# Optimization experiments

Hardware: AMD Instinct MI355X
Metric: run time of the kernel (lower is better)

The kernel has to match this reference:

```python
import jax, jax.numpy as jnp
import numpy as np

NUM_CLASSES = 512  # P distinct identities in the batch (labels are in [0, P))
TAU = 0.5
EPS = 1e-12


def _l2norm(x):
    # F.normalize(x, dim=1) with eps clamp
    n = jnp.sqrt(jnp.sum(x * x, axis=1, keepdims=True))
    return x / jnp.maximum(n, EPS)


def setup_inputs() -> dict:
    key = jax.random.key(0)
    k1, k2, k3 = jax.random.split(key, 3)
    N, D, P = 8192, 2048, NUM_CLASSES
    feat_vp = jax.random.normal(k1, (N, D), dtype=jnp.float32)
    feat_ap = jax.random.normal(k2, (N, D), dtype=jnp.float32)
    feat_rp = jax.random.normal(k3, (N, D), dtype=jnp.float32)
    # P identities, K = N/P instances each; every class present
    label = (jnp.arange(N) % P).astype(jnp.int32)
    return {"feat_vp": feat_vp, "feat_ap": feat_ap, "feat_rp": feat_rp, "label": label}


def reference(feat_vp, feat_ap, feat_rp, label):
    P = NUM_CLASSES
    fv = _l2norm(feat_vp)
    fa = _l2norm(feat_ap)
    fr = _l2norm(feat_rp)

    # segment-mean over labels (replaces the O(N^2 D) python loop)
    counts = jax.ops.segment_sum(jnp.ones_like(label, dtype=fv.dtype), label,
                                 num_segments=P)  # [P]
    inv_cnt = 1.0 / counts[:, None]

    def centers(f):
        s = jax.ops.segment_sum(f, label, num_segments=P)  # [P, D]
        return _l2norm(s * inv_cnt)

    cv, ca, cr = centers(fv), centers(fa), centers(fr)

    # per-sample centers = unique centers gathered back by label
    loss_intra = (jnp.sum((fv - cv[label]) ** 2, axis=1).mean()
                  + jnp.sum((fa - ca[label]) ** 2, axis=1).mean()
                  + jnp.sum((fr - cr[label]) ** 2, axis=1).mean())

    def pair_loss(c1, c2):
        logits = (c1 @ c2.T) / TAU  # [P, P]
        logp = jax.nn.log_softmax(logits, axis=1)
        return -jnp.mean(jnp.diagonal(logp))

    loss_inter = pair_loss(cv, ca) + pair_loss(cv, cr) + pair_loss(ca, cr)
    return loss_intra + loss_inter
```

## Files before the change

### kernel.cpp

```cpp
#include <hip/hip_runtime.h>
#include <hip/hip_bf16.h>

#define P_CLS 512
#define D_DIM 2048
#define CAP   32
#define CHUNK 8
#define TAU_INV 2.0f

typedef short short8 __attribute__((ext_vector_type(8)));
typedef float f32x4 __attribute__((ext_vector_type(4)));

__device__ __forceinline__ float wave_red_sum(float v) {
#pragma unroll
  for (int o = 32; o > 0; o >>= 1) v += __shfl_down(v, o, 64);
  return v;
}
__device__ __forceinline__ float wave_red_max(float v) {
#pragma unroll
  for (int o = 32; o > 0; o >>= 1) v = fmaxf(v, __shfl_down(v, o, 64));
  return v;
}

__global__ void k_init(int* cnt, float* accs) {
  int t = blockIdx.x * blockDim.x + threadIdx.x;
  if (t < P_CLS) cnt[t] = 0;
  if (t < 8) accs[t] = 0.f;
}

__global__ void k_index(const int* __restrict__ label, int* __restrict__ cnt,
                        int* __restrict__ idx, int n) {
  int i = blockIdx.x * blockDim.x + threadIdx.x;
  if (i < n) {
    int p = label[i];
    int slot = atomicAdd(&cnt[p], 1);
    if (slot < CAP) idx[p * CAP + slot] = i;
  }
}

__global__ __launch_bounds__(256)
void k_centers(const float* __restrict__ f0, const float* __restrict__ f1,
               const float* __restrict__ f2, const int* __restrict__ cnt,
               const int* __restrict__ idx, __hip_bfloat16* __restrict__ cb,
               float* __restrict__ accs) {
  __shared__ float red[4 * CHUNK];
  int p = blockIdx.x, m = blockIdx.y;
  const float* F = (m == 0) ? f0 : (m == 1) ? f1 : f2;
  int t = threadIdx.x;
  int lane = t & 63, wv = t >> 6;
  int c = cnt[p];
  if (c > CAP) c = CAP;
  const int* idxp = idx + p * CAP;
  f32x4 a0 = {0.f, 0.f, 0.f, 0.f}, a1 = {0.f, 0.f, 0.f, 0.f};
  for (int base = 0; base < c; base += CHUNK) {
    f32x4 v0[CHUNK], v1[CHUNK];
    float ssq[CHUNK];
#pragma unroll
    for (int r = 0; r < CHUNK; ++r) {
      int rr = base + r; if (rr >= c) rr = c - 1;
      long row = idxp[rr];
      const f32x4* src = (const f32x4*)(F + row * D_DIM);
      v0[r] = src[t];
      v1[r] = src[t + 256];
      f32x4 q0 = v0[r] * v0[r], q1 = v1[r] * v1[r];
      ssq[r] = q0.x + q0.y + q0.z + q0.w + q1.x + q1.y + q1.z + q1.w;
    }
    __syncthreads();
#pragma unroll
    for (int r = 0; r < CHUNK; ++r) {
      float v = wave_red_sum(ssq[r]);
      if (lane == 0) red[wv * CHUNK + r] = v;
    }
    __syncthreads();
#pragma unroll
    for (int r = 0; r < CHUNK; ++r) {
      float s = red[r] + red[CHUNK + r] + red[2 * CHUNK + r] + red[3 * CHUNK + r];
      float w = (base + r < c) ? (1.0f / fmaxf(sqrtf(s), 1e-12f)) : 0.0f;
      a0 += v0[r] * w;
      a1 += v1[r] * w;
    }
  }
  f32x4 q0 = a0 * a0, q1 = a1 * a1;
  float loc = q0.x + q0.y + q0.z + q0.w + q1.x + q1.y + q1.z + q1.w;
  loc = wave_red_sum(loc);
  __syncthreads();
  if (lane == 0) red[wv] = loc;
  __syncthreads();
  float snorm = sqrtf(red[0] + red[1] + red[2] + red[3]);
  float inv = 1.0f / fmaxf(snorm, 1e-12f);
  __hip_bfloat16* dst = cb + ((long)m * P_CLS + p) * D_DIM;
  int c0 = t * 4, c1 = D_DIM / 2 + t * 4;
  dst[c0 + 0] = __float2bfloat16(a0.x * inv);
  dst[c0 + 1] = __float2bfloat16(a0.y * inv);
  dst[c0 + 2] = __float2bfloat16(a0.z * inv);
  dst[c0 + 3] = __float2bfloat16(a0.w * inv);
  dst[c1 + 0] = __float2bfloat16(a1.x * inv);
  dst[c1 + 1] = __float2bfloat16(a1.y * inv);
  dst[c1 + 2] = __float2bfloat16(a1.z * inv);
  dst[c1 + 3] = __float2bfloat16(a1.w * inv);
  if (t == 0) atomicAdd(&accs[0], snorm);
}

__global__ __launch_bounds__(256)
void k_gemm(const __hip_bfloat16* __restrict__ cbh, float* __restrict__ logits) {
  __shared__ __align__(16) unsigned short As[64 * 40], Bs[64 * 40];
  int pair = blockIdx.y;
  int ma = (pair == 2) ? 1 : 0;
  int mb = (pair == 0) ? 1 : 2;
  const unsigned short* A = (const unsigned short*)cbh + (long)ma * P_CLS * D_DIM;
  const unsigned short* B = (const unsigned short*)cbh + (long)mb * P_CLS * D_DIM;
  float* C = logits + (long)pair * P_CLS * P_CLS;
  int tm = (blockIdx.x >> 3) * 64;
  int tn = (blockIdx.x & 7) * 64;
  int t = threadIdx.x, lane = t & 63, wv = t >> 6;
  int srow = t >> 2, skc = (t & 3) * 8;
  int quad = lane >> 4, mr = lane & 15;
  f32x4 acc[4] = {{0,0,0,0},{0,0,0,0},{0,0,0,0},{0,0,0,0}};
  for (int k0 = 0; k0 < D_DIM; k0 += 32) {
    uint4 av = *(const uint4*)(A + (long)(tm + srow) * D_DIM + k0 + skc);
    uint4 bv = *(const uint4*)(B + (long)(tn + srow) * D_DIM + k0 + skc);
    __syncthreads();
    *(uint4*)(As + srow * 40 + skc) = av;
    *(uint4*)(Bs + srow * 40 + skc) = bv;
    __syncthreads();
    short8 af = *(const short8*)(As + (wv * 16 + mr) * 40 + quad * 8);
#pragma unroll
    for (int nb = 0; nb < 4; ++nb) {
      short8 bfr = *(const short8*)(Bs + (nb * 16 + mr) * 40 + quad * 8);
      acc[nb] = __builtin_amdgcn_mfma_f32_16x16x32_bf16(af, bfr, acc[nb], 0, 0, 0);
    }
  }
  int crow = tm + wv * 16 + quad * 4;
#pragma unroll
  for (int nb = 0; nb < 4; ++nb)
#pragma unroll
    for (int r = 0; r < 4; ++r)
      C[(long)(crow + r) * P_CLS + tn + nb * 16 + mr] = acc[nb][r] * TAU_INV;
}

__global__ __launch_bounds__(256)
void k_lse(const float* __restrict__ logits, float* __restrict__ accs) {
  __shared__ float sred[8];
  int row = blockIdx.x;
  int p = row & (P_CLS - 1);
  const float* L = logits + (long)row * P_CLS;
  int t = threadIdx.x, lane = t & 63, wv = t >> 6;
  float v0 = L[t], v1 = L[t + 256];
  float mx = wave_red_max(fmaxf(v0, v1));
  if (lane == 0) sred[wv] = mx;
  __syncthreads();
  mx = fmaxf(fmaxf(sred[0], sred[1]), fmaxf(sred[2], sred[3]));
  float e = expf(v0 - mx) + expf(v1 - mx);
  e = wave_red_sum(e);
  if (lane == 0) sred[4 + wv] = e;
  __syncthreads();
  if (t == 0) {
    float tot = sred[4] + sred[5] + sred[6] + sred[7];
    atomicAdd(&accs[1], mx + logf(tot) - L[p]);
  }
}

__global__ void k_final(const float* __restrict__ accs, float* __restrict__ out,
                        float invN) {
  out[0] = 6.0f - 2.0f * invN * accs[0] + accs[1] * (1.0f / (float)P_CLS);
}

extern "C" void kernel_launch(void* const* d_in, const int* in_sizes, int n_in,
                              void* d_out, int out_size, void* d_ws, size_t ws_size,
                              hipStream_t stream) {
  const float* fvp = (const float*)d_in[0];
  const float* fap = (const float*)d_in[1];
  const float* frp = (const float*)d_in[2];
  const int* label = (const int*)d_in[3];
  int N = in_sizes[3];

  char* ws = (char*)d_ws;
  int* cnt = (int*)ws;
  int* idx = (int*)(ws + 2048);
  float* accs = (float*)(ws + 2048 + 65536);
  __hip_bfloat16* cb = (__hip_bfloat16*)(ws + 131072);
  float* logits = (float*)(ws + 131072 + 3ul * P_CLS * D_DIM * 2);

  hipLaunchKernelGGL(k_init, dim3(1), dim3(512), 0, stream, cnt, accs);
  hipLaunchKernelGGL(k_index, dim3((N + 255) / 256), dim3(256), 0, stream,
                     label, cnt, idx, N);
  hipLaunchKernelGGL(k_centers, dim3(P_CLS, 3), dim3(256), 0, stream,
                     fvp, fap, frp, cnt, idx, cb, accs);
  hipLaunchKernelGGL(k_gemm, dim3(64, 3), dim3(256), 0, stream, cb, logits);
  hipLaunchKernelGGL(k_lse, dim3(3 * P_CLS), dim3(256), 0, stream, logits, accs);
  hipLaunchKernelGGL(k_final, dim3(1), dim3(1), 0, stream, accs, (float*)d_out,
                     1.0f / (float)N);
}
```

Baseline: 258.1 us.

## Use one wave per center with row prefetch, split-K double-buffered GEMM

The center kernel now assigns one 64-lane wave per class, streaming rows with a one-row register prefetch and wave-only xor reductions. This removes the block-level syncs and shared-memory reductions, and it writes bf16 output as packed 8-byte stores. The GEMM is split over K into two partial logit buffers with double-buffered LDS and a two-deep register prefetch. The LSE kernel sums the two partials. Together these aim to raise GEMM occupancy and hide load latency, at the cost of extra logits memory traffic and an extra read in the LSE kernel.

```diff
diff --git a/kernel.cpp b/kernel.cpp
--- a/kernel.cpp
+++ b/kernel.cpp
@@ -4,20 +4,26 @@
 #define P_CLS 512
 #define D_DIM 2048
 #define CAP   32
-#define CHUNK 8
 #define TAU_INV 2.0f
 
 typedef short short8 __attribute__((ext_vector_type(8)));
 typedef float f32x4 __attribute__((ext_vector_type(4)));
 
-__device__ __forceinline__ float wave_red_sum(float v) {
-#pragma unroll
-  for (int o = 32; o > 0; o >>= 1) v += __shfl_down(v, o, 64);
+__device__ __forceinline__ unsigned short f2bf_bits(float x) {
+  __hip_bfloat16 b = __float2bfloat16(x);
+  unsigned short u;
+  __builtin_memcpy(&u, &b, sizeof(u));
+  return u;
+}
+
+__device__ __forceinline__ float xred_sum(float v) {
+#pragma unroll
+  for (int o = 1; o < 64; o <<= 1) v += __shfl_xor(v, o, 64);
   return v;
 }
-__device__ __forceinline__ float wave_red_max(float v) {
-#pragma unroll
-  for (int o = 32; o > 0; o >>= 1) v = fmaxf(v, __shfl_down(v, o, 64));
+__device__ __forceinline__ float xred_max(float v) {
+#pragma unroll
+  for (int o = 1; o < 64; o <<= 1) v = fmaxf(v, __shfl_xor(v, o, 64));
   return v;
 }
 
@@ -37,95 +43,106 @@
   }
 }
 
-__global__ __launch_bounds__(256)
+__global__ __launch_bounds__(128)
 void k_centers(const float* __restrict__ f0, const float* __restrict__ f1,
                const float* __restrict__ f2, const int* __restrict__ cnt,
                const int* __restrict__ idx, __hip_bfloat16* __restrict__ cb,
                float* __restrict__ accs) {
-  __shared__ float red[4 * CHUNK];
-  int p = blockIdx.x, m = blockIdx.y;
+  int wv = threadIdx.x >> 6, lane = threadIdx.x & 63;
+  int p = blockIdx.x * 2 + wv;
+  int m = blockIdx.y;
   const float* F = (m == 0) ? f0 : (m == 1) ? f1 : f2;
-  int t = threadIdx.x;
-  int lane = t & 63, wv = t >> 6;
   int c = cnt[p];
   if (c > CAP) c = CAP;
   const int* idxp = idx + p * CAP;
-  f32x4 a0 = {0.f, 0.f, 0.f, 0.f}, a1 = {0.f, 0.f, 0.f, 0.f};
-  for (int base = 0; base < c; base += CHUNK) {
-    f32x4 v0[CHUNK], v1[CHUNK];
-    float ssq[CHUNK];
-#pragma unroll
-    for (int r = 0; r < CHUNK; ++r) {
-      int rr = base + r; if (rr >= c) rr = c - 1;
-      long row = idxp[rr];
-      const f32x4* src = (const f32x4*)(F + row * D_DIM);
-      v0[r] = src[t];
-      v1[r] = src[t + 256];
-      f32x4 q0 = v0[r] * v0[r], q1 = v1[r] * v1[r];
-      ssq[r] = q0.x + q0.y + q0.z + q0.w + q1.x + q1.y + q1.z + q1.w;
-    }
-    __syncthreads();
-#pragma unroll
-    for (int r = 0; r < CHUNK; ++r) {
-      float v = wave_red_sum(ssq[r]);
-      if (lane == 0) red[wv * CHUNK + r] = v;
-    }
-    __syncthreads();
-#pragma unroll
-    for (int r = 0; r < CHUNK; ++r) {
-      float s = red[r] + red[CHUNK + r] + red[2 * CHUNK + r] + red[3 * CHUNK + r];
-      float w = (base + r < c) ? (1.0f / fmaxf(sqrtf(s), 1e-12f)) : 0.0f;
-      a0 += v0[r] * w;
-      a1 += v1[r] * w;
-    }
-  }
-  f32x4 q0 = a0 * a0, q1 = a1 * a1;
-  float loc = q0.x + q0.y + q0.z + q0.w + q1.x + q1.y + q1.z + q1.w;
-  loc = wave_red_sum(loc);
-  __syncthreads();
-  if (lane == 0) red[wv] = loc;
-  __syncthreads();
-  float snorm = sqrtf(red[0] + red[1] + red[2] + red[3]);
-  float inv = 1.0f / fmaxf(snorm, 1e-12f);
   __hip_bfloat16* dst = cb + ((long)m * P_CLS + p) * D_DIM;
-  int c0 = t * 4, c1 = D_DIM / 2 + t * 4;
-  dst[c0 + 0] = __float2bfloat16(a0.x * inv);
-  dst[c0 + 1] = __float2bfloat16(a0.y * inv);
-  dst[c0 + 2] = __float2bfloat16(a0.z * inv);
-  dst[c0 + 3] = __float2bfloat16(a0.w * inv);
-  dst[c1 + 0] = __float2bfloat16(a1.x * inv);
-  dst[c1 + 1] = __float2bfloat16(a1.y * inv);
-  dst[c1 + 2] = __float2bfloat16(a1.z * inv);
-  dst[c1 + 3] = __float2bfloat16(a1.w * inv);
-  if (t == 0) atomicAdd(&accs[0], snorm);
+
+  f32x4 acc[8] = {};
+  if (c > 0) {
+    f32x4 v[8], nv[8];
+    const f32x4* rp = (const f32x4*)(F + (long)idxp[0] * D_DIM);
+#pragma unroll
+    for (int k = 0; k < 8; ++k) v[k] = rp[lane + k * 64];
+    for (int r = 0; r < c; ++r) {
+      if (r + 1 < c) {
+        const f32x4* np = (const f32x4*)(F + (long)idxp[r + 1] * D_DIM);
+#pragma unroll
+        for (int k = 0; k < 8; ++k) nv[k] = np[lane + k * 64];
+      }
+      float ssq = 0.f;
+#pragma unroll
+      for (int k = 0; k < 8; ++k) {
+        f32x4 q = v[k] * v[k];
+        ssq += q.x + q.y + q.z + q.w;
+      }
+      ssq = xred_sum(ssq);
+      float w = 1.0f / fmaxf(sqrtf(ssq), 1e-12f);
+#pragma unroll
+      for (int k = 0; k < 8; ++k) acc[k] += v[k] * w;
+#pragma unroll
+      for (int k = 0; k < 8; ++k) v[k] = nv[k];
+    }
+  }
+  float s2 = 0.f;
+#pragma unroll
+  for (int k = 0; k < 8; ++k) {
+    f32x4 q = acc[k] * acc[k];
+    s2 += q.x + q.y + q.z + q.w;
+  }
+  s2 = xred_sum(s2);
+  float sn = sqrtf(s2);
+  float inv = 1.0f / fmaxf(sn, 1e-12f);
+#pragma unroll
+  for (int k = 0; k < 8; ++k) {
+    f32x4 o = acc[k] * inv;
+    ushort4 h;
+    h.x = f2bf_bits(o.x);
+    h.y = f2bf_bits(o.y);
+    h.z = f2bf_bits(o.z);
+    h.w = f2bf_bits(o.w);
+    ((ushort4*)dst)[lane + k * 64] = h;
+  }
+  if (lane == 0 && c > 0) atomicAdd(&accs[0], sn);
 }
 
 __global__ __launch_bounds__(256)
 void k_gemm(const __hip_bfloat16* __restrict__ cbh, float* __restrict__ logits) {
-  __shared__ __align__(16) unsigned short As[64 * 40], Bs[64 * 40];
-  int pair = blockIdx.y;
+  __shared__ __align__(16) unsigned short As[2][64 * 40], Bs[2][64 * 40];
+  int pair = blockIdx.y, kz = blockIdx.z;
   int ma = (pair == 2) ? 1 : 0;
   int mb = (pair == 0) ? 1 : 2;
-  const unsigned short* A = (const unsigned short*)cbh + (long)ma * P_CLS * D_DIM;
-  const unsigned short* B = (const unsigned short*)cbh + (long)mb * P_CLS * D_DIM;
-  float* C = logits + (long)pair * P_CLS * P_CLS;
-  int tm = (blockIdx.x >> 3) * 64;
-  int tn = (blockIdx.x & 7) * 64;
+  const unsigned short* A =
+      (const unsigned short*)cbh + (long)ma * P_CLS * D_DIM + kz * (D_DIM / 2);
+  const unsigned short* B =
+      (const unsigned short*)cbh + (long)mb * P_CLS * D_DIM + kz * (D_DIM / 2);
+  float* C = logits + ((long)kz * 3 + pair) * P_CLS * P_CLS;
+  int tm = (blockIdx.x >> 3) * 64, tn = (blockIdx.x & 7) * 64;
   int t = threadIdx.x, lane = t & 63, wv = t >> 6;
   int srow = t >> 2, skc = (t & 3) * 8;
   int quad = lane >> 4, mr = lane & 15;
+  const unsigned short* pa = A + (long)(tm + srow) * D_DIM + skc;
+  const unsigned short* pb = B + (long)(tn + srow) * D_DIM + skc;
   f32x4 acc[4] = {{0,0,0,0},{0,0,0,0},{0,0,0,0},{0,0,0,0}};
-  for (int k0 = 0; k0 < D_DIM; k0 += 32) {
-    uint4 av = *(const uint4*)(A + (long)(tm + srow) * D_DIM + k0 + skc);
-    uint4 bv = *(const uint4*)(B + (long)(tn + srow) * D_DIM + k0 + skc);
+  uint4 av = *(const uint4*)pa, bv = *(const uint4*)pb;
+  *(uint4*)(&As[0][srow * 40 + skc]) = av;
+  *(uint4*)(&Bs[0][srow * 40 + skc]) = bv;
+  av = *(const uint4*)(pa + 32); bv = *(const uint4*)(pb + 32);
+  const int NIT = (D_DIM / 2) / 32;
+  for (int it = 0; it < NIT; ++it) {
     __syncthreads();
-    *(uint4*)(As + srow * 40 + skc) = av;
-    *(uint4*)(Bs + srow * 40 + skc) = bv;
-    __syncthreads();
-    short8 af = *(const short8*)(As + (wv * 16 + mr) * 40 + quad * 8);
+    int cur = it & 1;
+    if (it + 1 < NIT) {
+      *(uint4*)(&As[cur ^ 1][srow * 40 + skc]) = av;
+      *(uint4*)(&Bs[cur ^ 1][srow * 40 + skc]) = bv;
+    }
+    if (it + 2 < NIT) {
+      av = *(const uint4*)(pa + (it + 2) * 32);
+      bv = *(const uint4*)(pb + (it + 2) * 32);
+    }
+    short8 af = *(const short8*)(&As[cur][(wv * 16 + mr) * 40 + quad * 8]);
 #pragma unroll
     for (int nb = 0; nb < 4; ++nb) {
-      short8 bfr = *(const short8*)(Bs + (nb * 16 + mr) * 40 + quad * 8);
+      short8 bfr = *(const short8*)(&Bs[cur][(nb * 16 + mr) * 40 + quad * 8]);
       acc[nb] = __builtin_amdgcn_mfma_f32_16x16x32_bf16(af, bfr, acc[nb], 0, 0, 0);
     }
   }
@@ -142,20 +159,23 @@
   __shared__ float sred[8];
   int row = blockIdx.x;
   int p = row & (P_CLS - 1);
-  const float* L = logits + (long)row * P_CLS;
+  const float* L0 = logits + (long)row * P_CLS;
+  const float* L1 = L0 + 3l * P_CLS * P_CLS;
   int t = threadIdx.x, lane = t & 63, wv = t >> 6;
-  float v0 = L[t], v1 = L[t + 256];
-  float mx = wave_red_max(fmaxf(v0, v1));
+  float v0 = L0[t] + L1[t];
+  float v1 = L0[t + 256] + L1[t + 256];
+  float mx = xred_max(fmaxf(v0, v1));
   if (lane == 0) sred[wv] = mx;
   __syncthreads();
   mx = fmaxf(fmaxf(sred[0], sred[1]), fmaxf(sred[2], sred[3]));
   float e = expf(v0 - mx) + expf(v1 - mx);
-  e = wave_red_sum(e);
+  e = xred_sum(e);
   if (lane == 0) sred[4 + wv] = e;
   __syncthreads();
   if (t == 0) {
     float tot = sred[4] + sred[5] + sred[6] + sred[7];
-    atomicAdd(&accs[1], mx + logf(tot) - L[p]);
+    float diag = L0[p] + L1[p];
+    atomicAdd(&accs[1], mx + logf(tot) - diag);
   }
 }
 
@@ -183,9 +203,9 @@
   hipLaunchKernelGGL(k_init, dim3(1), dim3(512), 0, stream, cnt, accs);
   hipLaunchKernelGGL(k_index, dim3((N + 255) / 256), dim3(256), 0, stream,
                      label, cnt, idx, N);
-  hipLaunchKernelGGL(k_centers, dim3(P_CLS, 3), dim3(256), 0, stream,
+  hipLaunchKernelGGL(k_centers, dim3(P_CLS / 2, 3), dim3(128), 0, stream,
                      fvp, fap, frp, cnt, idx, cb, accs);
-  hipLaunchKernelGGL(k_gemm, dim3(64, 3), dim3(256), 0, stream, cb, logits);
+  hipLaunchKernelGGL(k_gemm, dim3(64, 3, 2), dim3(256), 0, stream, cb, logits);
   hipLaunchKernelGGL(k_lse, dim3(3 * P_CLS), dim3(256), 0, stream, logits, accs);
   hipLaunchKernelGGL(k_final, dim3(1), dim3(1), 0, stream, accs, (float*)d_out,
                      1.0f / (float)N);
```

Result: faster. 249.0 us (-3.5%).
